# Optimization experiments

Hardware: AMD Instinct MI355X
Metric: run time of the kernel (lower is better)

## Reference

```python
import jax, jax.numpy as jnp
import numpy as np

D_MODEL = 1024
N_HEADS = 16
HEAD_DIM = D_MODEL // N_HEADS
ROPE_BASE = 10000.0
RMS_EPS = 1e-5


def setup_inputs() -> dict:
    key = jax.random.key(0)
    k1, k2, k3 = jax.random.split(key, 3)
    B, T = 2, 2048
    x = jax.random.normal(k1, (B, T, D_MODEL), dtype=jnp.float32)
    norm_w = jnp.ones((D_MODEL,), dtype=jnp.float32)
    w_qkv = jax.random.normal(k2, (3 * D_MODEL, D_MODEL), dtype=jnp.float32) * (D_MODEL ** -0.5)
    w_out = jax.random.normal(k3, (D_MODEL, D_MODEL), dtype=jnp.float32) * (D_MODEL ** -0.5)
    return {"x": x, "norm_w": norm_w, "w_qkv": w_qkv, "w_out": w_out}


def _rope_cos_sin(T, dtype):
    inv_freq = 1.0 / (ROPE_BASE ** (jnp.arange(0, HEAD_DIM, 2, dtype=jnp.float32) / HEAD_DIM))
    t = jnp.arange(T, dtype=jnp.float32)
    freqs = t[:, None] * inv_freq[None, :]            # [T, HEAD_DIM//2]
    emb = jnp.concatenate([freqs, freqs], axis=-1)    # [T, HEAD_DIM]
    return jnp.cos(emb).astype(dtype), jnp.sin(emb).astype(dtype)


def _rotate_half(x):
    x1, x2 = jnp.split(x, 2, axis=-1)
    return jnp.concatenate([-x2, x1], axis=-1)


def reference(x, norm_w, w_qkv, w_out):
    B, T, _ = x.shape
    residual = x
    # RMSNorm
    rms = jax.lax.rsqrt(jnp.mean(x * x, axis=-1, keepdims=True) + RMS_EPS)
    xn = x * rms * norm_w
    # QKV projection (torch Linear: x @ W.T)
    qkv = xn @ w_qkv.T                                  # [B, T, 3*D]
    qkv = qkv.reshape(B, T, 3, N_HEADS, HEAD_DIM)
    q, k, v = qkv[:, :, 0], qkv[:, :, 1], qkv[:, :, 2]  # [B, T, H, hd]
    # RoPE on q, k
    cos, sin = _rope_cos_sin(T, q.dtype)                # [T, hd]
    cos = cos[None, :, None, :]
    sin = sin[None, :, None, :]
    q = q * cos + _rotate_half(q) * sin
    k = k * cos + _rotate_half(k) * sin
    # Bidirectional SDPA: [B, H, T, hd]
    qh = q.transpose(0, 2, 1, 3)
    kh = k.transpose(0, 2, 1, 3)
    vh = v.transpose(0, 2, 1, 3)
    scale = HEAD_DIM ** -0.5
    scores = jnp.einsum('bhqd,bhkd->bhqk', qh, kh) * scale
    attn = jax.nn.softmax(scores, axis=-1)
    out = jnp.einsum('bhqk,bhkd->bhqd', attn, vh)       # [B, H, T, hd]
    out = out.transpose(0, 2, 1, 3).reshape(B, T, D_MODEL)
    out = out @ w_out.T
    return residual + out
```

## Files before the change

### kernel.cpp

```cpp
#include <hip/hip_runtime.h>
#include <hip/hip_bf16.h>
#include <math.h>


typedef __bf16 bf16;
typedef __bf16 bf16x8 __attribute__((ext_vector_type(8)));
typedef __bf16 bf16x4 __attribute__((ext_vector_type(4)));
typedef float  f32x4  __attribute__((ext_vector_type(4)));
typedef unsigned u32x4 __attribute__((ext_vector_type(4)));

#define GLOAD16(g, l) __builtin_amdgcn_global_load_lds( \
    (const __attribute__((address_space(1))) void*)(g),  \
    (__attribute__((address_space(3))) void*)(l), 16, 0, 0)

__device__ __forceinline__ unsigned pk2(float a, float b) {
  unsigned short lo = __builtin_bit_cast(unsigned short, (bf16)a);
  unsigned short hi = __builtin_bit_cast(unsigned short, (bf16)b);
  return (unsigned)lo | ((unsigned)hi << 16);
}

__global__ __launch_bounds__(256) void k_cvt(const float* __restrict__ src,
    bf16* __restrict__ dst, int n) {
  int i = (blockIdx.x * 256 + threadIdx.x) * 8;
  if (i >= n) return;
  float4 a = *(const float4*)(src + i);
  float4 b = *(const float4*)(src + i + 4);
  bf16x8 o;
  o[0] = (bf16)a.x; o[1] = (bf16)a.y; o[2] = (bf16)a.z; o[3] = (bf16)a.w;
  o[4] = (bf16)b.x; o[5] = (bf16)b.y; o[6] = (bf16)b.z; o[7] = (bf16)b.w;
  *(bf16x8*)(dst + i) = o;
}

__global__ __launch_bounds__(256) void k_rmsnorm(const float* __restrict__ x,
    const float* __restrict__ w, bf16* __restrict__ xn) {
  const int row = blockIdx.x, tid = threadIdx.x;
  float4 v = *(const float4*)(x + (size_t)row * 1024 + tid * 4);
  float ss = v.x * v.x + v.y * v.y + v.z * v.z + v.w * v.w;
  for (int m = 32; m >= 1; m >>= 1) ss += __shfl_xor(ss, m);
  __shared__ float red[4];
  if ((tid & 63) == 0) red[tid >> 6] = ss;
  __syncthreads();
  float ms = (red[0] + red[1] + red[2] + red[3]) * (1.f / 1024.f);
  float r = rsqrtf(ms + 1e-5f);
  float4 wv = *(const float4*)(w + tid * 4);
  bf16x4 o;
  o[0] = (bf16)(v.x * r * wv.x); o[1] = (bf16)(v.y * r * wv.y);
  o[2] = (bf16)(v.z * r * wv.z); o[3] = (bf16)(v.w * r * wv.w);
  *(bf16x4*)(xn + (size_t)row * 1024 + tid * 4) = o;
}

template<int RESID, int TM>
__global__ __launch_bounds__(256, 2) void k_gemm_bt(const bf16* __restrict__ A,
    const bf16* __restrict__ B, const float* __restrict__ R, void* __restrict__ Cv,
    int M, int N, int K, int lda) {
  constexpr int MT = TM / 32;
  constexpr int AELEM = TM * 64;
  constexpr int SMEM = (AELEM + 8192 > TM * 136) ? (AELEM + 8192) : (TM * 136);
  const int tid = threadIdx.x;
  const int lane = tid & 63, L15 = lane & 15, quad = lane >> 4;
  const int wave = tid >> 6, wr = wave >> 1, wc = wave & 1;
  const int n0 = blockIdx.x * 128, m0 = blockIdx.y * TM;
  __shared__ __align__(16) bf16 smem[SMEM];
  bf16* sA = smem; bf16* sB = smem + AELEM;
  f32x4 acc[MT][4];
  const f32x4 z = {0.f, 0.f, 0.f, 0.f};
  for (int i = 0; i < MT; i++) for (int j = 0; j < 4; j++) acc[i][j] = z;

  for (int k0 = 0; k0 < K; k0 += 64) {
    const bf16* Ab = A + (size_t)m0 * lda + k0;
    const bf16* Bb = B + (size_t)n0 * K + k0;
    for (int p = 0; p < TM / 32; p++) {
      int s = p * 256 + tid, r = s >> 3, c8 = (s & 7) ^ (r & 7);
      GLOAD16(Ab + (size_t)r * lda + c8 * 8, sA + s * 8);
    }
    for (int p = 0; p < 4; p++) {
      int s = p * 256 + tid, r = s >> 3, c8 = (s & 7) ^ (r & 7);
      GLOAD16(Bb + (size_t)r * K + c8 * 8, sB + s * 8);
    }
    __syncthreads();
    for (int kk = 0; kk < 2; kk++) {
      bf16x8 af[MT], bfv[4];
      for (int i = 0; i < MT; i++) {
        int ra = wr * (TM / 2) + i * 16 + L15;
        af[i] = *(const bf16x8*)(sA + ra * 64 + (((kk * 4 + quad) ^ (ra & 7)) * 8));
      }
      for (int i = 0; i < 4; i++) {
        int rb = wc * 64 + i * 16 + L15;
        bfv[i] = *(const bf16x8*)(sB + rb * 64 + (((kk * 4 + quad) ^ (rb & 7)) * 8));
      }
      for (int mt = 0; mt < MT; mt++)
        for (int nt = 0; nt < 4; nt++)
          acc[mt][nt] = __builtin_amdgcn_mfma_f32_16x16x32_bf16(af[mt], bfv[nt], acc[mt][nt], 0, 0, 0);
    }
    __syncthreads();
  }
  bf16* sC = smem;
  for (int mt = 0; mt < MT; mt++) for (int nt = 0; nt < 4; nt++) {
    int r = wr * (TM / 2) + mt * 16 + quad * 4, c = wc * 64 + nt * 16 + L15;
    f32x4 v = acc[mt][nt];
    for (int g = 0; g < 4; g++) sC[(r + g) * 136 + c] = (bf16)v[g];
  }
  __syncthreads();
  constexpr int TPR = 256 / TM;
  constexpr int CPT = 128 / TPR;
  const int rr = tid / TPR, sg = (tid % TPR) * CPT;
  const size_t row = (size_t)m0 + rr;
  const bf16* src = sC + rr * 136 + sg;
  if (RESID) {
    float* Cf = (float*)Cv;
    const float* rs = R + row * N + n0 + sg;
    float* dst = Cf + row * N + n0 + sg;
    for (int i = 0; i < CPT / 4; i++) {
      bf16x4 u = *(const bf16x4*)(src + i * 4);
      float4 rv = *(const float4*)(rs + i * 4);
      float4 o;
      o.x = (float)u[0] + rv.x; o.y = (float)u[1] + rv.y;
      o.z = (float)u[2] + rv.z; o.w = (float)u[3] + rv.w;
      *(float4*)(dst + i * 4) = o;
    }
  } else {
    bf16* Cb = (bf16*)Cv;
    bf16* dst = Cb + row * N + n0 + sg;
    for (int i = 0; i < CPT / 8; i++)
      *(bf16x8*)(dst + i * 8) = *(const bf16x8*)(src + i * 8);
  }
}

__global__ __launch_bounds__(256) void k_rope(bf16* __restrict__ qkv,
    bf16* __restrict__ vt) {
  const int blk = blockIdx.x;
  const int tt = blk & 31, h = (blk >> 5) & 15, b = blk >> 9;
  const int tid = threadIdx.x;
  const int bh = b * 16 + h;
  {
    const int tl = tid >> 2, dp = (tid & 3) * 8;
    const int tg = tt * 64 + tl;
    bf16* base = qkv + (size_t)(b * 2048 + tg) * 3072 + h * 64;
    bf16x8 qlo = *(const bf16x8*)(base + dp);
    bf16x8 qhi = *(const bf16x8*)(base + dp + 32);
    bf16x8 klo = *(const bf16x8*)(base + 1024 + dp);
    bf16x8 khi = *(const bf16x8*)(base + 1024 + dp + 32);
    bf16x8 oql, oqh, okl, okh;
    for (int j = 0; j < 8; j++) {
      float invf = exp2f(-0.41524101186f * (float)(dp + j));
      float th = (float)tg * invf;
      float sn, cs;
      sincosf(th, &sn, &cs);
      float a0 = (float)qlo[j], a1 = (float)qhi[j];
      float b0 = (float)klo[j], b1 = (float)khi[j];
      oql[j] = (bf16)(a0 * cs - a1 * sn);
      oqh[j] = (bf16)(a1 * cs + a0 * sn);
      okl[j] = (bf16)(b0 * cs - b1 * sn);
      okh[j] = (bf16)(b1 * cs + b0 * sn);
    }
    *(bf16x8*)(base + dp) = oql; *(bf16x8*)(base + dp + 32) = oqh;
    *(bf16x8*)(base + 1024 + dp) = okl; *(bf16x8*)(base + 1024 + dp + 32) = okh;
  }
  __shared__ __align__(16) bf16 sT[64 * 72];
  for (int p = 0; p < 2; p++) {
    int s = p * 256 + tid, tl = s >> 3, c = s & 7;
    const bf16* vsrc = qkv + (size_t)(b * 2048 + tt * 64 + tl) * 3072 + 2048 + h * 64 + c * 8;
    *(bf16x8*)(sT + tl * 72 + c * 8) = *(const bf16x8*)vsrc;
  }
  __syncthreads();
  for (int p = 0; p < 2; p++) {
    int s = p * 256 + tid, d = s >> 3, tc = s & 7;
    bf16x8 v;
    for (int j = 0; j < 8; j++) v[j] = sT[(tc * 8 + j) * 72 + d];
    *(bf16x8*)(vt + (size_t)bh * 131072 + (size_t)d * 2048 + tt * 64 + tc * 8) = v;
  }
}

__global__ __launch_bounds__(512, 4) void k_attn(bf16* __restrict__ qkv,
    const bf16* __restrict__ vt) {
  const int tid = threadIdx.x;
  const int lane = tid & 63, L15 = lane & 15, quad = lane >> 4;
  const int wave = tid >> 6;
  const int bh = blockIdx.y, b = bh >> 4, h = bh & 15;
  const int q0 = blockIdx.x * 128;
  const bf16* Q  = qkv + (size_t)b * 2048 * 3072 + h * 64;
  const bf16* Kg = qkv + (size_t)b * 2048 * 3072 + 1024 + h * 64;
  const bf16* Vg = vt + (size_t)bh * 131072;
  __shared__ __align__(16) bf16 smem[32768];

  bf16x8 qf[2];
  {
    int rq = q0 + wave * 16 + L15;
    for (int kk = 0; kk < 2; kk++)
      qf[kk] = *(const bf16x8*)(Q + (size_t)rq * 3072 + kk * 32 + quad * 8);
  }
  f32x4 o[4];
  const f32x4 z = {0.f, 0.f, 0.f, 0.f};
  for (int i = 0; i < 4; i++) o[i] = z;
  f32x4 o5 = z;
  const bf16 one = (bf16)1.0f;
  const bf16x8 ones8 = {one, one, one, one, one, one, one, one};
  const float c2l = 0.125f * 1.44269504089f;
  const float mc  = 5.0f * 1.44269504089f;

  auto STAGE = [&](int kv0, int base) {
    const bf16* Kb = Kg + (size_t)kv0 * 3072;
    bf16* sKb = smem + base;
    bf16* sVb = smem + base + 8192;
    for (int p = 0; p < 2; p++) {
      int s = p * 512 + tid, r = s >> 3, c8 = (s & 7) ^ (r & 7);
      GLOAD16(Kb + (size_t)r * 3072 + c8 * 8, sKb + s * 8);
    }
    for (int p = 0; p < 2; p++) {
      int s = p * 512 + tid, r = s >> 4, cl = s & 15;
      int c8 = (cl & 8) | ((cl ^ (r & 7)) & 7);
      GLOAD16(Vg + (size_t)r * 2048 + kv0 + c8 * 8, sVb + s * 8);
    }
  };

  STAGE(0, 0);
  for (int t = 0; t < 16; ++t) {
    const int cur = (t & 1) << 14;
    if (t < 15) {
      STAGE((t + 1) << 7, cur ^ 16384);
      asm volatile("s_waitcnt vmcnt(4)" ::: "memory");
    } else {
      asm volatile("s_waitcnt vmcnt(0)" ::: "memory");
    }
    __builtin_amdgcn_s_barrier();
    __builtin_amdgcn_sched_barrier(0);
    const bf16* sK = smem + cur;
    const bf16* sV = smem + cur + 8192;

    f32x4 st[8];
#pragma unroll
    for (int i = 0; i < 8; i++) st[i] = z;
#pragma unroll
    for (int kk = 0; kk < 2; kk++) {
      bf16x8 kf[8];
#pragma unroll
      for (int kvt = 0; kvt < 8; kvt++) {
        int rk = kvt * 16 + L15;
        kf[kvt] = *(const bf16x8*)(sK + rk * 64 + (((kk * 4 + quad) ^ (rk & 7)) * 8));
      }
      __builtin_amdgcn_s_setprio(1);
#pragma unroll
      for (int kvt = 0; kvt < 8; kvt++)
        st[kvt] = __builtin_amdgcn_mfma_f32_16x16x32_bf16(kf[kvt], qf[kk], st[kvt], 0, 0, 0);
      __builtin_amdgcn_s_setprio(0);
    }
    unsigned pA[8], pB[8];
#pragma unroll
    for (int kvt = 0; kvt < 8; kvt++) {
      float p0 = __builtin_amdgcn_exp2f(st[kvt][0] * c2l - mc);
      float p1 = __builtin_amdgcn_exp2f(st[kvt][1] * c2l - mc);
      float p2 = __builtin_amdgcn_exp2f(st[kvt][2] * c2l - mc);
      float p3 = __builtin_amdgcn_exp2f(st[kvt][3] * c2l - mc);
      pA[kvt] = pk2(p0, p1);
      pB[kvt] = pk2(p2, p3);
    }
#pragma unroll
    for (int kc = 0; kc < 4; kc++) {
      bf16x8 vf[4];
#pragma unroll
      for (int dt = 0; dt < 4; dt++) {
        int rd = dt * 16 + L15;
        int c = kc * 4 + quad;
        int cs = (c & 8) | ((c ^ (rd & 7)) & 7);
        vf[dt] = *(const bf16x8*)(sV + rd * 128 + cs * 8);
      }
      auto rA = __builtin_amdgcn_permlane32_swap(pA[2 * kc], pA[2 * kc + 1], false, false);
      auto tAC = __builtin_amdgcn_permlane16_swap(rA[0], rA[1], false, false);
      auto rB = __builtin_amdgcn_permlane32_swap(pB[2 * kc], pB[2 * kc + 1], false, false);
      auto tBD = __builtin_amdgcn_permlane16_swap(rB[0], rB[1], false, false);
      u32x4 pw;
      pw[0] = tAC[0]; pw[1] = tBD[0]; pw[2] = tAC[1]; pw[3] = tBD[1];
      bf16x8 pf = __builtin_bit_cast(bf16x8, pw);
      __builtin_amdgcn_s_setprio(1);
#pragma unroll
      for (int dt = 0; dt < 4; dt++)
        o[dt] = __builtin_amdgcn_mfma_f32_16x16x32_bf16(vf[dt], pf, o[dt], 0, 0, 0);
      o5 = __builtin_amdgcn_mfma_f32_16x16x32_bf16(ones8, pf, o5, 0, 0, 0);
      __builtin_amdgcn_s_setprio(0);
    }
    asm volatile("s_waitcnt lgkmcnt(0)" ::: "memory");
    __builtin_amdgcn_sched_barrier(0);
    __builtin_amdgcn_s_barrier();
  }
  float invl = 1.f / o5[0];
  bf16* sO = smem;
  for (int dt = 0; dt < 4; dt++) {
    f32x4 v = o[dt] * invl;
    int ql = wave * 16 + L15;
    uint2 w2; w2.x = pk2(v[0], v[1]); w2.y = pk2(v[2], v[3]);
    *(uint2*)(sO + ql * 72 + dt * 16 + quad * 4) = w2;
  }
  __syncthreads();
  const int rr = tid >> 2, sg = (tid & 3) * 16;
  const bf16* src = sO + rr * 72 + sg;
  bf16* dst = qkv + (size_t)(b * 2048 + q0 + rr) * 3072 + h * 64 + sg;
  for (int i = 0; i < 2; i++)
    *(bf16x8*)(dst + i * 8) = *(const bf16x8*)(src + i * 8);
}

extern "C" void kernel_launch(void* const* d_in, const int* in_sizes, int n_in,
                              void* d_out, int out_size, void* d_ws, size_t ws_size,
                              hipStream_t stream) {
  (void)in_sizes; (void)n_in; (void)out_size;
  const float* x     = (const float*)d_in[0];
  const float* normw = (const float*)d_in[1];
  const float* wqkv  = (const float*)d_in[2];
  const float* wout  = (const float*)d_in[3];
  float* out = (float*)d_out;
  bf16* ws  = (bf16*)d_ws;
  const size_t NQKV = (size_t)4096 * 3072, NXN = (size_t)4096 * 1024;
  const size_t NWQ = (size_t)3072 * 1024, NWO = (size_t)1024 * 1024;
  const size_t need = (NQKV + NXN + NWQ + NWO) * sizeof(bf16);
  if (ws_size < need) return;
  bf16* qkv    = ws;
  bf16* xn     = qkv + NQKV;
  bf16* vtp    = xn;
  bf16* wqkvb  = xn + NXN;
  bf16* woutb  = wqkvb + NWQ;
  k_cvt<<<(int)(NWQ / 8 / 256), 256, 0, stream>>>(wqkv, wqkvb, (int)NWQ);
  k_cvt<<<(int)(NWO / 8 / 256), 256, 0, stream>>>(wout, woutb, (int)NWO);
  k_rmsnorm<<<4096, 256, 0, stream>>>(x, normw, xn);
  k_gemm_bt<0, 128><<<dim3(24, 32), 256, 0, stream>>>(xn, wqkvb, nullptr, qkv, 4096, 3072, 1024, 1024);
  k_rope<<<1024, 256, 0, stream>>>(qkv, vtp);
  k_attn<<<dim3(16, 32), 512, 0, stream>>>(qkv, vtp);
  k_gemm_bt<1, 64><<<dim3(8, 64), 256, 0, stream>>>(qkv, woutb, x, out, 4096, 1024, 1024, 3072);
}
```

Baseline: 201.1 us.

## Fuse RoPE into QKV GEMM epilogue using precomputed cos/sin table

Result: faster. 195.1 us (-3.0%).

```diff
diff --git a/kernel.cpp b/kernel.cpp
--- a/kernel.cpp
+++ b/kernel.cpp
@@ -29,6 +29,16 @@
   o[0] = (bf16)a.x; o[1] = (bf16)a.y; o[2] = (bf16)a.z; o[3] = (bf16)a.w;
   o[4] = (bf16)b.x; o[5] = (bf16)b.y; o[6] = (bf16)b.z; o[7] = (bf16)b.w;
   *(bf16x8*)(dst + i) = o;
+}
+
+__global__ __launch_bounds__(256) void k_tab(float2* __restrict__ tab) {
+  int idx = blockIdx.x * 256 + threadIdx.x;
+  int t = idx >> 5, j = idx & 31;
+  float invf = exp2f(-0.41524101186f * (float)j);
+  float th = (float)t * invf;
+  float sn, cs;
+  sincosf(th, &sn, &cs);
+  tab[idx] = make_float2(cs, sn);
 }
 
 __global__ __launch_bounds__(256) void k_rmsnorm(const float* __restrict__ x,
@@ -49,10 +59,11 @@
   *(bf16x4*)(xn + (size_t)row * 1024 + tid * 4) = o;
 }
 
-template<int RESID, int TM>
-__global__ __launch_bounds__(256, 2) void k_gemm_bt(const bf16* __restrict__ A,
-    const bf16* __restrict__ B, const float* __restrict__ R, void* __restrict__ Cv,
-    int M, int N, int K, int lda) {
+template<int RESID, int TM, int ROPE>
+__global__ __launch_bounds__(256, (TM == 128) ? 3 : 2) void k_gemm_bt(
+    const bf16* __restrict__ A, const bf16* __restrict__ B,
+    const float* __restrict__ R, void* __restrict__ Cv,
+    int M, int N, int K, int lda, const float2* __restrict__ tab) {
   constexpr int MT = TM / 32;
   constexpr int AELEM = TM * 64;
   constexpr int SMEM = (AELEM + 8192 > TM * 136) ? (AELEM + 8192) : (TM * 136);
@@ -88,11 +99,28 @@
         int rb = wc * 64 + i * 16 + L15;
         bfv[i] = *(const bf16x8*)(sB + rb * 64 + (((kk * 4 + quad) ^ (rb & 7)) * 8));
       }
+      __builtin_amdgcn_s_setprio(1);
       for (int mt = 0; mt < MT; mt++)
         for (int nt = 0; nt < 4; nt++)
           acc[mt][nt] = __builtin_amdgcn_mfma_f32_16x16x32_bf16(af[mt], bfv[nt], acc[mt][nt], 0, 0, 0);
+      __builtin_amdgcn_s_setprio(0);
     }
     __syncthreads();
+  }
+  if (ROPE && (n0 >> 10) < 2) {
+    const int tb = (m0 & 2047) + wr * (TM / 2);
+    for (int mt = 0; mt < MT; mt++) {
+      for (int nt = 0; nt < 2; nt++) {
+        const int j = nt * 16 + L15;
+        for (int g = 0; g < 4; g++) {
+          int t = tb + mt * 16 + quad * 4 + g;
+          float2 cs = tab[t * 32 + j];
+          float lo = acc[mt][nt][g], hi = acc[mt][nt + 2][g];
+          acc[mt][nt][g]     = lo * cs.x - hi * cs.y;
+          acc[mt][nt + 2][g] = hi * cs.x + lo * cs.y;
+        }
+      }
+    }
   }
   bf16* sC = smem;
   for (int mt = 0; mt < MT; mt++) for (int nt = 0; nt < 4; nt++) {
@@ -126,36 +154,12 @@
   }
 }
 
-__global__ __launch_bounds__(256) void k_rope(bf16* __restrict__ qkv,
+__global__ __launch_bounds__(256) void k_vt(const bf16* __restrict__ qkv,
     bf16* __restrict__ vt) {
   const int blk = blockIdx.x;
   const int tt = blk & 31, h = (blk >> 5) & 15, b = blk >> 9;
   const int tid = threadIdx.x;
   const int bh = b * 16 + h;
-  {
-    const int tl = tid >> 2, dp = (tid & 3) * 8;
-    const int tg = tt * 64 + tl;
-    bf16* base = qkv + (size_t)(b * 2048 + tg) * 3072 + h * 64;
-    bf16x8 qlo = *(const bf16x8*)(base + dp);
-    bf16x8 qhi = *(const bf16x8*)(base + dp + 32);
-    bf16x8 klo = *(const bf16x8*)(base + 1024 + dp);
-    bf16x8 khi = *(const bf16x8*)(base + 1024 + dp + 32);
-    bf16x8 oql, oqh, okl, okh;
-    for (int j = 0; j < 8; j++) {
-      float invf = exp2f(-0.41524101186f * (float)(dp + j));
-      float th = (float)tg * invf;
-      float sn, cs;
-      sincosf(th, &sn, &cs);
-      float a0 = (float)qlo[j], a1 = (float)qhi[j];
-      float b0 = (float)klo[j], b1 = (float)khi[j];
-      oql[j] = (bf16)(a0 * cs - a1 * sn);
-      oqh[j] = (bf16)(a1 * cs + a0 * sn);
-      okl[j] = (bf16)(b0 * cs - b1 * sn);
-      okh[j] = (bf16)(b1 * cs + b0 * sn);
-    }
-    *(bf16x8*)(base + dp) = oql; *(bf16x8*)(base + dp + 32) = oqh;
-    *(bf16x8*)(base + 1024 + dp) = okl; *(bf16x8*)(base + 1024 + dp + 32) = okh;
-  }
   __shared__ __align__(16) bf16 sT[64 * 72];
   for (int p = 0; p < 2; p++) {
     int s = p * 256 + tid, tl = s >> 3, c = s & 7;
@@ -317,11 +321,13 @@
   bf16* vtp    = xn;
   bf16* wqkvb  = xn + NXN;
   bf16* woutb  = wqkvb + NWQ;
+  float2* tab  = (float2*)out;
   k_cvt<<<(int)(NWQ / 8 / 256), 256, 0, stream>>>(wqkv, wqkvb, (int)NWQ);
   k_cvt<<<(int)(NWO / 8 / 256), 256, 0, stream>>>(wout, woutb, (int)NWO);
+  k_tab<<<256, 256, 0, stream>>>(tab);
   k_rmsnorm<<<4096, 256, 0, stream>>>(x, normw, xn);
-  k_gemm_bt<0, 128><<<dim3(24, 32), 256, 0, stream>>>(xn, wqkvb, nullptr, qkv, 4096, 3072, 1024, 1024);
-  k_rope<<<1024, 256, 0, stream>>>(qkv, vtp);
+  k_gemm_bt<0, 128, 1><<<dim3(24, 32), 256, 0, stream>>>(xn, wqkvb, nullptr, qkv, 4096, 3072, 1024, 1024, tab);
+  k_vt<<<1024, 256, 0, stream>>>(qkv, vtp);
   k_attn<<<dim3(16, 32), 512, 0, stream>>>(qkv, vtp);
-  k_gemm_bt<1, 64><<<dim3(8, 64), 256, 0, stream>>>(qkv, woutb, x, out, 4096, 1024, 1024, 3072);
-}
+  k_gemm_bt<1, 64, 0><<<dim3(8, 64), 256, 0, stream>>>(qkv, woutb, x, out, 4096, 1024, 1024, 3072, nullptr);
+}
```
